# Kernel optimization log

Measured on AMD Instinct MI355X. Metric: run time of the kernel, lower is better.

The kernel has to match this reference:

```python
import jax, jax.numpy as jnp
import numpy as np

N, E, B = 8192, 32768, 64      # nodes, edges, graphs
NF, EF, D, OUT = 32, 16, 64, 12
T_MP = 3                        # MPNN message-passing steps (Gilmer et al.)
T_S2S = 12                      # Set2Set processing steps


def setup_inputs() -> dict:
    key = jax.random.key(0)
    ks = jax.random.split(key, 16)
    g = lambda i, shape, fan_in: jax.random.normal(ks[i], shape, jnp.float32) * (fan_in ** -0.5)
    return {
        "node_features": jax.random.normal(ks[0], (N, NF), jnp.float32),
        "edge_features": jax.random.normal(ks[1], (E, EF), jnp.float32),
        "Esrc": jax.random.randint(ks[2], (E,), 0, N),
        "Etgt": jax.random.randint(ks[3], (E,), 0, N),
        "batch": jnp.sort(jax.random.randint(ks[4], (N,), 0, B)),
        # input projection
        "W_in": g(5, (NF, D), NF), "b_in": jnp.zeros((D,), jnp.float32),
        # edge encoder MLP -> per-edge DxD matrix
        "W_ee1": g(6, (EF, D), EF), "b_ee1": jnp.zeros((D,), jnp.float32),
        "W_ee2": g(7, (D, D * D), D), "b_ee2": jnp.zeros((D * D,), jnp.float32),
        # GRU cell (node update)
        "W_ih": g(8, (D, 3 * D), D), "W_hh": g(9, (D, 3 * D), D),
        "b_ih": jnp.zeros((3 * D,), jnp.float32), "b_hh": jnp.zeros((3 * D,), jnp.float32),
        # Set2Set LSTM cell (input 2D, hidden D)
        "Wl_ih": g(10, (2 * D, 4 * D), 2 * D), "Wl_hh": g(11, (D, 4 * D), D),
        "bl_ih": jnp.zeros((4 * D,), jnp.float32), "bl_hh": jnp.zeros((4 * D,), jnp.float32),
        # output head
        "W_out": g(12, (D, OUT), D), "b_out": jnp.zeros((OUT,), jnp.float32),
    }


def reference(node_features, edge_features, Esrc, Etgt, batch,
              W_in, b_in, W_ee1, b_ee1, W_ee2, b_ee2,
              W_ih, W_hh, b_ih, b_hh, Wl_ih, Wl_hh, bl_ih, bl_hh,
              W_out, b_out):
    # EdgeEncoderMLP: edge features -> per-edge [D, D] message transform
    ed = jax.nn.relu(edge_features @ W_ee1 + b_ee1)
    A = (ed @ W_ee2 + b_ee2).reshape(E, D, D)
    x = node_features @ W_in + b_in          # [N, D]

    def gru(h, m):
        gi = m @ W_ih + b_ih
        gh = h @ W_hh + b_hh
        ir, iz, i_n = jnp.split(gi, 3, axis=-1)
        hr, hz, h_n = jnp.split(gh, 3, axis=-1)
        r = jax.nn.sigmoid(ir + hr)
        z = jax.nn.sigmoid(iz + hz)
        n = jnp.tanh(i_n + r * h_n)
        return (1.0 - z) * n + z * h

    def mp_step(h, _):
        msg = jnp.einsum('eij,ej->ei', A, h[Esrc])          # gather + edge-conditioned transform
        agg = jax.ops.segment_sum(msg, Etgt, num_segments=N)  # scatter-add
        return gru(h, agg), None

    x, _ = jax.lax.scan(mp_step, x, None, length=T_MP)       # [N, D]

    # Set2Set attentive pooling
    def lstm(h, c, q_star):
        gates = q_star @ Wl_ih + bl_ih + h @ Wl_hh + bl_hh
        i, f, g_, o = jnp.split(gates, 4, axis=-1)
        c = jax.nn.sigmoid(f) * c + jax.nn.sigmoid(i) * jnp.tanh(g_)
        h = jax.nn.sigmoid(o) * jnp.tanh(c)
        return h, c

    def s2s_step(carry, _):
        h, c, q_star = carry
        h, c = lstm(h, c, q_star)
        q = h                                                # [B, D]
        e = jnp.sum(x * q[batch], axis=-1)                   # [N]
        emax = jax.lax.stop_gradient(jax.ops.segment_max(e, batch, num_segments=B))
        ex = jnp.exp(e - emax[batch])
        denom = jax.ops.segment_sum(ex, batch, num_segments=B)
        a = ex / denom[batch]                                # segment softmax
        r = jax.ops.segment_sum(a[:, None] * x, batch, num_segments=B)  # [B, D]
        return (h, c, jnp.concatenate([q, r], axis=-1)), None

    zD = jnp.zeros((B, D), x.dtype)
    (_, _, q_star), _ = jax.lax.scan(
        s2s_step, (zD, zD, jnp.zeros((B, 2 * D), x.dtype)), None, length=T_S2S)

    return q_star[:, :D] @ W_out + b_out
```

## Files before the change

kernel.cpp:

```cpp
#include <hip/hip_runtime.h>

#define N_NODES 8192
#define N_EDGES 32768
#define N_GRAPHS 64
#define D 64
#define D2 4096
#define NF 32
#define EF 16
#define OUTF 12
#define T_MP 3
#define T_S2S 12
#define MAXN 224
#define ETILES 16

typedef unsigned short u16;
typedef _Float16 f16;
typedef __attribute__((ext_vector_type(8))) _Float16 f16x8;
typedef __attribute__((ext_vector_type(8))) unsigned short ushort8;
typedef __attribute__((ext_vector_type(4))) float f32x4;

__device__ inline float sigm(float x) { return 1.0f / (1.0f + __expf(-x)); }
__device__ inline float tanhe(float x) { float e = __expf(2.f * x); return 1.f - 2.f / (e + 1.f); }

__global__ void k_node_proj(const float* __restrict__ nf, const float* __restrict__ W_in,
                            const float* __restrict__ b_in, float* __restrict__ h) {
    int id = blockIdx.x * 256 + threadIdx.x;
    int n = id >> 6, d = id & 63;
    float acc = b_in[d];
#pragma unroll
    for (int k = 0; k < NF; ++k) acc += nf[n * NF + k] * W_in[k * D + d];
    h[id] = acc;
}

__global__ void k_edge_mlp(const float* __restrict__ ef, const float* __restrict__ W1,
                           const float* __restrict__ b1, f16* __restrict__ ed16) {
    int id = blockIdx.x * 256 + threadIdx.x;
    int e = id >> 6, d = id & 63;
    float acc = b1[d];
#pragma unroll
    for (int k = 0; k < EF; ++k) acc += ef[e * EF + k] * W1[k * D + d];
    ed16[id] = (f16)fmaxf(acc, 0.f);
}

__global__ void k_cvt_w2t(const float* __restrict__ W2, f16* __restrict__ W2T) {
    int id = blockIdx.x * 256 + threadIdx.x;
    int c = id >> 6, k = id & 63;
    W2T[id] = (f16)W2[(size_t)k * D2 + c];
}

__global__ void k_csr_count(const int* __restrict__ Etgt, int* __restrict__ cnt) {
    int e = blockIdx.x * 256 + threadIdx.x;
    atomicAdd(&cnt[Etgt[e]], 1);
}
__global__ void k_csr_scan(const int* __restrict__ cnt, int* __restrict__ rowptr,
                           int* __restrict__ cursor, const int* __restrict__ batch,
                           int* __restrict__ row_start) {
    __shared__ int part[256];
    int t = threadIdx.x;
    if (t <= N_GRAPHS) {
        int lo = 0, hi = N_NODES;
        while (lo < hi) { int mid = (lo + hi) >> 1; if (batch[mid] < t) lo = mid + 1; else hi = mid; }
        row_start[t] = lo;
    }
    int loc[32];
    int s = 0;
#pragma unroll
    for (int k = 0; k < 32; ++k) { loc[k] = s; s += cnt[t * 32 + k]; }
    part[t] = s;
    __syncthreads();
    if (t == 0) {
        int a = 0;
        for (int i = 0; i < 256; ++i) { int v = part[i]; part[i] = a; a += v; }
        rowptr[N_NODES] = a;
    }
    __syncthreads();
    int b = part[t];
#pragma unroll
    for (int k = 0; k < 32; ++k) {
        rowptr[t * 32 + k] = b + loc[k];
        cursor[t * 32 + k] = b + loc[k];
    }
}
__global__ void k_csr_place(const int* __restrict__ Etgt, int* __restrict__ cursor,
                            int* __restrict__ eidx) {
    int e = blockIdx.x * 256 + threadIdx.x;
    int t = Etgt[e];
    int pos = atomicAdd(&cursor[t], 1);
    eidx[pos] = e;
}

__global__ void __launch_bounds__(256, 2)
k_mp_step(const f16* __restrict__ ed16, const f16* __restrict__ w2t,
          const float* __restrict__ h, const int* __restrict__ Esrc,
          float* __restrict__ msg) {
    __shared__ __attribute__((aligned(16))) char lds[2][6144];
    int tid = threadIdx.x;
    int wv = tid >> 6, lane = tid & 63;
    int g4 = lane >> 4, r15 = lane & 15;
    int ibase = blockIdx.y * 16 + wv * 4;
    int e_base = blockIdx.x * (16 * ETILES);
    f16x8 wf[4][4][2];
#pragma unroll
    for (int ii = 0; ii < 4; ++ii)
#pragma unroll
        for (int jt = 0; jt < 4; ++jt) {
            size_t roff = (size_t)((ibase + ii) * D + jt * 16 + r15) * D + g4 * 8;
            wf[ii][jt][0] = *(const f16x8*)(w2t + roff);
            wf[ii][jt][1] = *(const f16x8*)(w2t + roff + 32);
        }
    const int hrow = tid >> 4, hch = tid & 15;
    const int erow = tid >> 3, ech = tid & 7;
#define MP_STAGE(tt, bb) do {                                                        \
        int eb_ = e_base + (tt) * 16;                                                \
        int src_ = Esrc[eb_ + hrow];                                                 \
        f32x4 hvv_ = *(const f32x4*)(h + (size_t)src_ * D + hch * 4);                \
        *(f32x4*)(lds[bb] + hrow * 256 + ((hch ^ hrow) << 4)) = hvv_;                \
        if (tid < 128) {                                                             \
            f16x8 ev_ = *(const f16x8*)(ed16 + (size_t)(eb_ + erow) * D + ech * 8);  \
            *(f16x8*)(lds[bb] + 4096 + erow * 128 + ((ech ^ (erow & 7)) << 4)) = ev_;\
        }                                                                            \
    } while (0)
    MP_STAGE(0, 0);
    for (int t = 0; t < ETILES; ++t) {
        __syncthreads();
        if (t + 1 < ETILES) {
            const int nb = (t + 1) & 1;
            if (nb) MP_STAGE(t + 1, 1); else MP_STAGE(t + 1, 0);
        }
        const char* buf = lds[t & 1];
        int sw = (r15 & 7) << 4;
        f32x4 hv[4];
#pragma unroll
        for (int jt = 0; jt < 4; ++jt)
            hv[jt] = *(const f32x4*)(buf + r15 * 256 + (((jt * 4 + g4) ^ r15) << 4));
        f16x8 e0 = *(const f16x8*)(buf + 4096 + r15 * 128 + ((g4 << 4) ^ sw));
        f16x8 e1 = *(const f16x8*)(buf + 4096 + r15 * 128 + (((g4 + 4) << 4) ^ sw));
        f32x4 acc[4][4];
#pragma unroll
        for (int ii = 0; ii < 4; ++ii)
#pragma unroll
            for (int jt = 0; jt < 4; ++jt) { acc[ii][jt][0]=0.f; acc[ii][jt][1]=0.f; acc[ii][jt][2]=0.f; acc[ii][jt][3]=0.f; }
#pragma unroll
        for (int ii = 0; ii < 4; ++ii)
#pragma unroll
            for (int jt = 0; jt < 4; ++jt)
                acc[ii][jt] = __builtin_amdgcn_mfma_f32_16x16x32_f16(wf[ii][jt][0], e0, acc[ii][jt], 0, 0, 0);
#pragma unroll
        for (int ii = 0; ii < 4; ++ii)
#pragma unroll
            for (int jt = 0; jt < 4; ++jt)
                acc[ii][jt] = __builtin_amdgcn_mfma_f32_16x16x32_f16(wf[ii][jt][1], e1, acc[ii][jt], 0, 0, 0);
        float p[4];
#pragma unroll
        for (int ii = 0; ii < 4; ++ii) {
            float s = 0.f;
#pragma unroll
            for (int jt = 0; jt < 4; ++jt)
#pragma unroll
                for (int r = 0; r < 4; ++r) s += acc[ii][jt][r] * hv[jt][r];
            s += __shfl_xor(s, 16);
            s += __shfl_xor(s, 32);
            p[ii] = s;
        }
        int e = e_base + t * 16 + r15;
#pragma unroll
        for (int ii = 0; ii < 4; ++ii)
            if (g4 == ii) msg[(size_t)e * D + ibase + ii] = p[ii];
    }
#undef MP_STAGE
}

__global__ void k_gru(const float* __restrict__ msg, const int* __restrict__ rowptr,
                      const int* __restrict__ eidx, const float* __restrict__ W_ih,
                      const float* __restrict__ W_hh, const float* __restrict__ b_ih,
                      const float* __restrict__ b_hh, float* __restrict__ h) {
    int id = blockIdx.x * 256 + threadIdx.x;
    int n = id >> 6, d = id & 63;
    float m_d = 0.f;
    int p0 = rowptr[n], p1 = rowptr[n + 1];
    for (int p = p0; p < p1; ++p) {
        int eid = eidx[p];
        m_d += msg[(size_t)eid * D + d];
    }
    float h_d = h[id];
    float ir = b_ih[d], iz = b_ih[D + d], in_ = b_ih[2 * D + d];
    float hr = b_hh[d], hz = b_hh[D + d], hn = b_hh[2 * D + d];
#pragma unroll 8
    for (int k = 0; k < D; ++k) {
        float mk = __shfl(m_d, k);
        float hk = __shfl(h_d, k);
        const float* wi = W_ih + k * 3 * D;
        const float* wh = W_hh + k * 3 * D;
        ir += mk * wi[d];      iz += mk * wi[D + d];      in_ += mk * wi[2 * D + d];
        hr += hk * wh[d];      hz += hk * wh[D + d];      hn  += hk * wh[2 * D + d];
    }
    float r = sigm(ir + hr), z = sigm(iz + hz);
    float nn = tanhf(in_ + r * hn);
    h[id] = (1.f - z) * nn + z * h_d;
}

__global__ void __launch_bounds__(256, 1)
k_set2set(const float* __restrict__ x, const int* __restrict__ row_start,
          const float* __restrict__ Wl_ih, const float* __restrict__ Wl_hh,
          const float* __restrict__ bl_ih, const float* __restrict__ bl_hh,
          const float* __restrict__ W_out, const float* __restrict__ b_out,
          float* __restrict__ out) {
    __shared__ __attribute__((aligned(16))) float x_lds[MAXN * D];
    __shared__ __attribute__((aligned(16))) float e_lds[MAXN];
    __shared__ __attribute__((aligned(16))) float h_s[D], c_s[D], qs[2 * D];
    __shared__ __attribute__((aligned(16))) float gates[4 * D], wr[4][D], wmaxs[4], wsexs[4];
    int g = blockIdx.x;
    int tid = threadIdx.x;
    int wave = tid >> 6, lane = tid & 63;
    int ns = row_start[g], ne = row_start[g + 1];
    int nloc = ne - ns;
    float bl = bl_ih[tid] + bl_hh[tid];
    for (int q = tid; q < nloc * 16; q += 256) {
        int n = q >> 4, c = q & 15;
        f32x4 v = *(const f32x4*)(x + (size_t)(ns + n) * D + c * 4);
        *(f32x4*)&x_lds[n * D + ((c ^ (n & 15)) << 2)] = v;
    }
    if (tid < D) { h_s[tid] = 0.f; c_s[tid] = 0.f; }
    if (tid < 2 * D) qs[tid] = 0.f;
    __syncthreads();
    for (int step = 0; step < T_S2S; ++step) {
        float a0 = bl, a1 = 0.f, a2 = 0.f, a3 = 0.f;
#pragma unroll
        for (int k = 0; k < 2 * D; k += 4) {
            f32x4 qv = *(const f32x4*)&qs[k];
            a0 += qv[0] * Wl_ih[(k + 0) * 256 + tid];
            a1 += qv[1] * Wl_ih[(k + 1) * 256 + tid];
            a2 += qv[2] * Wl_ih[(k + 2) * 256 + tid];
            a3 += qv[3] * Wl_ih[(k + 3) * 256 + tid];
        }
#pragma unroll
        for (int k = 0; k < D; k += 4) {
            f32x4 hvv = *(const f32x4*)&h_s[k];
            a0 += hvv[0] * Wl_hh[(k + 0) * 256 + tid];
            a1 += hvv[1] * Wl_hh[(k + 1) * 256 + tid];
            a2 += hvv[2] * Wl_hh[(k + 2) * 256 + tid];
            a3 += hvv[3] * Wl_hh[(k + 3) * 256 + tid];
        }
        gates[tid] = (a0 + a1) + (a2 + a3);
        __syncthreads();
        if (tid < D) {
            float ig = sigm(gates[tid]),          fg = sigm(gates[D + tid]);
            float gg = tanhe(gates[2 * D + tid]), og = sigm(gates[3 * D + tid]);
            float cn = fg * c_s[tid] + ig * gg;
            c_s[tid] = cn;
            h_s[tid] = og * tanhe(cn);
        }
        __syncthreads();
        float e_val = -INFINITY;
        int n = tid;
        if (n < nloc) {
            float d0 = 0.f, d1 = 0.f, d2 = 0.f, d3 = 0.f;
#pragma unroll
            for (int c = 0; c < 16; ++c) {
                f32x4 xv = *(const f32x4*)&x_lds[n * D + ((c ^ (n & 15)) << 2)];
                d0 += xv[0] * h_s[c * 4];     d1 += xv[1] * h_s[c * 4 + 1];
                d2 += xv[2] * h_s[c * 4 + 2]; d3 += xv[3] * h_s[c * 4 + 3];
            }
            e_val = (d0 + d1) + (d2 + d3);
        }
        float wm = e_val;
#pragma unroll
        for (int m = 1; m < 64; m <<= 1) wm = fmaxf(wm, __shfl_xor(wm, m));
        if (lane == 0) wmaxs[wave] = wm;
        __syncthreads();
        float gmax = fmaxf(fmaxf(wmaxs[0], wmaxs[1]), fmaxf(wmaxs[2], wmaxs[3]));
        if (n < nloc) e_lds[n] = __expf(e_val - gmax);
        __syncthreads();
        float racc = 0.f, sex = 0.f;
        for (int nn = wave; nn < nloc; nn += 4) {
            int c = lane >> 2, w = lane & 3;
            float xv = x_lds[nn * D + ((c ^ (nn & 15)) << 2) + w];
            float ex = e_lds[nn];
            racc += ex * xv;
            sex += ex;
        }
        wr[wave][lane] = racc;
        if (lane == 0) wsexs[wave] = sex;
        __syncthreads();
        if (tid < D) {
            float denom = wsexs[0] + wsexs[1] + wsexs[2] + wsexs[3];
            float r = wr[0][tid] + wr[1][tid] + wr[2][tid] + wr[3][tid];
            r = (denom > 0.f) ? r / denom : 0.f;
            qs[tid] = h_s[tid];
            qs[D + tid] = r;
        }
        __syncthreads();
    }
    if (tid < OUTF) {
        float acc = b_out[tid];
        for (int d = 0; d < D; ++d) acc += h_s[d] * W_out[d * OUTF + tid];
        out[g * OUTF + tid] = acc;
    }
}

extern "C" void kernel_launch(void* const* d_in, const int* in_sizes, int n_in,
                              void* d_out, int out_size, void* d_ws, size_t ws_size,
                              hipStream_t stream) {
    const float* node_features = (const float*)d_in[0];
    const float* edge_features = (const float*)d_in[1];
    const int*   Esrc  = (const int*)d_in[2];
    const int*   Etgt  = (const int*)d_in[3];
    const int*   batch = (const int*)d_in[4];
    const float* W_in  = (const float*)d_in[5];
    const float* b_in  = (const float*)d_in[6];
    const float* W_ee1 = (const float*)d_in[7];
    const float* b_ee1 = (const float*)d_in[8];
    const float* W_ee2 = (const float*)d_in[9];
    const float* W_ih  = (const float*)d_in[11];
    const float* W_hh  = (const float*)d_in[12];
    const float* b_ih  = (const float*)d_in[13];
    const float* b_hh  = (const float*)d_in[14];
    const float* Wl_ih = (const float*)d_in[15];
    const float* Wl_hh = (const float*)d_in[16];
    const float* bl_ih = (const float*)d_in[17];
    const float* bl_hh = (const float*)d_in[18];
    const float* W_out = (const float*)d_in[19];
    const float* b_out = (const float*)d_in[20];

    char* ws = (char*)d_ws;
    float* h        = (float*)(ws);
    float* msg      = (float*)(ws + (size_t)(2 << 20));
    f16*   ed16     = (f16*)  (ws + (size_t)(10 << 20));
    f16*   w2t      = (f16*)  (ws + (size_t)(18 << 20));
    int*   rowptr   = (int*)  (ws + (size_t)(19 << 20));
    int*   cursor   = (int*)  (ws + (size_t)(19 << 20) + (64 << 10));
    int*   eidx     = (int*)  (ws + (size_t)(19 << 20) + (128 << 10));
    int*   row_start= (int*)  (ws + (size_t)(19 << 20) + (512 << 10));
    const size_t REQUIRED = (size_t)(20 << 20);
    if (ws_size < REQUIRED) return;

    k_node_proj<<<N_NODES * D / 256, 256, 0, stream>>>(node_features, W_in, b_in, h);
    k_edge_mlp <<<N_EDGES * D / 256, 256, 0, stream>>>(edge_features, W_ee1, b_ee1, ed16);
    k_cvt_w2t  <<<D2 * D / 256, 256, 0, stream>>>(W_ee2, w2t);
    hipMemsetAsync(cursor, 0, N_NODES * sizeof(int), stream);
    k_csr_count<<<N_EDGES / 256, 256, 0, stream>>>(Etgt, cursor);
    k_csr_scan <<<1, 256, 0, stream>>>(cursor, rowptr, cursor, batch, row_start);
    k_csr_place<<<N_EDGES / 256, 256, 0, stream>>>(Etgt, cursor, eidx);
    for (int t = 0; t < T_MP; ++t) {
        k_mp_step<<<dim3(N_EDGES / (16 * ETILES), D / 16), 256, 0, stream>>>(
            ed16, w2t, h, Esrc, msg);
        k_gru<<<N_NODES * D / 256, 256, 0, stream>>>(msg, rowptr, eidx, W_ih, W_hh, b_ih, b_hh, h);
    }
    k_set2set<<<N_GRAPHS, 256, 0, stream>>>(h, row_start, Wl_ih, Wl_hh, bl_ih, bl_hh,
                                            W_out, b_out, (float*)d_out);
}
```

Before: 279.3 us.

## Fuse prologue kernels and stage GRU weights in LDS with larger blocks

Merges the node projection, edge MLP and W2 conversion into a single launch that dispatches work by block index, removing two kernel launches. The GRU kernel now runs 1024-thread blocks covering 16 nodes, copying W_ih and W_hh (96KB total) into shared memory before the gate matmuls so weight reads come from LDS rather than global/L2. The trade-off is a per-block weight copy plus a barrier, and with 96KB of LDS and launch_bounds(1024,1) each CU holds fewer resident blocks to hide the gather latency.

```diff
diff --git a/kernel.cpp b/kernel.cpp
--- a/kernel.cpp
+++ b/kernel.cpp
@@ -22,30 +22,31 @@
 __device__ inline float sigm(float x) { return 1.0f / (1.0f + __expf(-x)); }
 __device__ inline float tanhe(float x) { float e = __expf(2.f * x); return 1.f - 2.f / (e + 1.f); }
 
-__global__ void k_node_proj(const float* __restrict__ nf, const float* __restrict__ W_in,
-                            const float* __restrict__ b_in, float* __restrict__ h) {
-    int id = blockIdx.x * 256 + threadIdx.x;
-    int n = id >> 6, d = id & 63;
-    float acc = b_in[d];
-#pragma unroll
-    for (int k = 0; k < NF; ++k) acc += nf[n * NF + k] * W_in[k * D + d];
-    h[id] = acc;
-}
-
-__global__ void k_edge_mlp(const float* __restrict__ ef, const float* __restrict__ W1,
-                           const float* __restrict__ b1, f16* __restrict__ ed16) {
-    int id = blockIdx.x * 256 + threadIdx.x;
-    int e = id >> 6, d = id & 63;
-    float acc = b1[d];
-#pragma unroll
-    for (int k = 0; k < EF; ++k) acc += ef[e * EF + k] * W1[k * D + d];
-    ed16[id] = (f16)fmaxf(acc, 0.f);
-}
-
-__global__ void k_cvt_w2t(const float* __restrict__ W2, f16* __restrict__ W2T) {
-    int id = blockIdx.x * 256 + threadIdx.x;
-    int c = id >> 6, k = id & 63;
-    W2T[id] = (f16)W2[(size_t)k * D2 + c];
+__global__ void k_prologue(const float* __restrict__ nf, const float* __restrict__ W_in,
+                           const float* __restrict__ b_in, float* __restrict__ h,
+                           const float* __restrict__ ef, const float* __restrict__ W1,
+                           const float* __restrict__ b1, f16* __restrict__ ed16,
+                           const float* __restrict__ W2, f16* __restrict__ W2T) {
+    int b = blockIdx.x, tid = threadIdx.x;
+    if (b < N_NODES * D / 256) {
+        int id = b * 256 + tid;
+        int n = id >> 6, d = id & 63;
+        float acc = b_in[d];
+#pragma unroll
+        for (int k = 0; k < NF; ++k) acc += nf[n * NF + k] * W_in[k * D + d];
+        h[id] = acc;
+    } else if (b < N_NODES * D / 256 + N_EDGES * D / 256) {
+        int id = (b - N_NODES * D / 256) * 256 + tid;
+        int e = id >> 6, d = id & 63;
+        float acc = b1[d];
+#pragma unroll
+        for (int k = 0; k < EF; ++k) acc += ef[e * EF + k] * W1[k * D + d];
+        ed16[id] = (f16)fmaxf(acc, 0.f);
+    } else {
+        int id = (b - N_NODES * D / 256 - N_EDGES * D / 256) * 256 + tid;
+        int c = id >> 6, k = id & 63;
+        W2T[id] = (f16)W2[(size_t)k * D2 + c];
+    }
 }
 
 __global__ void k_csr_count(const int* __restrict__ Etgt, int* __restrict__ cnt) {
@@ -170,12 +171,21 @@
 #undef MP_STAGE
 }
 
-__global__ void k_gru(const float* __restrict__ msg, const int* __restrict__ rowptr,
-                      const int* __restrict__ eidx, const float* __restrict__ W_ih,
-                      const float* __restrict__ W_hh, const float* __restrict__ b_ih,
-                      const float* __restrict__ b_hh, float* __restrict__ h) {
-    int id = blockIdx.x * 256 + threadIdx.x;
-    int n = id >> 6, d = id & 63;
+__global__ void __launch_bounds__(1024, 1)
+k_gru(const float* __restrict__ msg, const int* __restrict__ rowptr,
+      const int* __restrict__ eidx, const float* __restrict__ W_ih,
+      const float* __restrict__ W_hh, const float* __restrict__ b_ih,
+      const float* __restrict__ b_hh, float* __restrict__ h) {
+    __shared__ __attribute__((aligned(16))) float wih_s[D * 3 * D];
+    __shared__ __attribute__((aligned(16))) float whh_s[D * 3 * D];
+    int tid = threadIdx.x;
+    for (int c = tid; c < 3072; c += 1024) {
+        ((f32x4*)wih_s)[c] = ((const f32x4*)W_ih)[c];
+        ((f32x4*)whh_s)[c] = ((const f32x4*)W_hh)[c];
+    }
+    int n = blockIdx.x * 16 + (tid >> 6);
+    int d = tid & 63;
+    int id = n * D + d;
     float m_d = 0.f;
     int p0 = rowptr[n], p1 = rowptr[n + 1];
     for (int p = p0; p < p1; ++p) {
@@ -183,14 +193,15 @@
         m_d += msg[(size_t)eid * D + d];
     }
     float h_d = h[id];
+    __syncthreads();
     float ir = b_ih[d], iz = b_ih[D + d], in_ = b_ih[2 * D + d];
     float hr = b_hh[d], hz = b_hh[D + d], hn = b_hh[2 * D + d];
 #pragma unroll 8
     for (int k = 0; k < D; ++k) {
         float mk = __shfl(m_d, k);
         float hk = __shfl(h_d, k);
-        const float* wi = W_ih + k * 3 * D;
-        const float* wh = W_hh + k * 3 * D;
+        const float* wi = wih_s + k * 3 * D;
+        const float* wh = whh_s + k * 3 * D;
         ir += mk * wi[d];      iz += mk * wi[D + d];      in_ += mk * wi[2 * D + d];
         hr += hk * wh[d];      hz += hk * wh[D + d];      hn  += hk * wh[2 * D + d];
     }
@@ -334,9 +345,8 @@
     const size_t REQUIRED = (size_t)(20 << 20);
     if (ws_size < REQUIRED) return;
 
-    k_node_proj<<<N_NODES * D / 256, 256, 0, stream>>>(node_features, W_in, b_in, h);
-    k_edge_mlp <<<N_EDGES * D / 256, 256, 0, stream>>>(edge_features, W_ee1, b_ee1, ed16);
-    k_cvt_w2t  <<<D2 * D / 256, 256, 0, stream>>>(W_ee2, w2t);
+    k_prologue<<<N_NODES * D / 256 + N_EDGES * D / 256 + D2 * D / 256, 256, 0, stream>>>(
+        node_features, W_in, b_in, h, edge_features, W_ee1, b_ee1, ed16, W_ee2, w2t);
     hipMemsetAsync(cursor, 0, N_NODES * sizeof(int), stream);
     k_csr_count<<<N_EDGES / 256, 256, 0, stream>>>(Etgt, cursor);
     k_csr_scan <<<1, 256, 0, stream>>>(cursor, rowptr, cursor, batch, row_start);
@@ -344,7 +354,7 @@
     for (int t = 0; t < T_MP; ++t) {
         k_mp_step<<<dim3(N_EDGES / (16 * ETILES), D / 16), 256, 0, stream>>>(
             ed16, w2t, h, Esrc, msg);
-        k_gru<<<N_NODES * D / 256, 256, 0, stream>>>(msg, rowptr, eidx, W_ih, W_hh, b_ih, b_hh, h);
+        k_gru<<<N_NODES / 16, 1024, 0, stream>>>(msg, rowptr, eidx, W_ih, W_hh, b_ih, b_hh, h);
     }
     k_set2set<<<N_GRAPHS, 256, 0, stream>>>(h, row_start, Wl_ih, Wl_hh, bl_ih, bl_hh,
                                             W_out, b_out, (float*)d_out);
```

Result: slower. 299.7 us (+7.3%).
